# Performance work log

Hardware: AMD Instinct MI355X
Metric: run time of the kernel (lower is better)

Reference implementation:

```python
import jax, jax.numpy as jnp
import numpy as np

NUM_TRAITS = 5
NUM_MODALITIES = 3
K = 8
EPS = 1e-08


def setup_inputs() -> dict:
    key = jax.random.key(0)
    k1, k2, k3, k4 = jax.random.split(key, 4)
    labeled_embeddings = jax.random.normal(k1, (20000, NUM_MODALITIES, 256), dtype=jnp.float32)
    labeled_traits = jax.random.uniform(k2, (20000, NUM_TRAITS), dtype=jnp.float32)
    unlabeled_embeddings = jax.random.normal(k3, (2048, NUM_MODALITIES, 256), dtype=jnp.float32)
    trait_modality_logits = jax.random.normal(k4, (NUM_TRAITS, NUM_MODALITIES), dtype=jnp.float32)
    return {
        'labeled_embeddings': labeled_embeddings,
        'labeled_traits': labeled_traits,
        'unlabeled_embeddings': unlabeled_embeddings,
        'trait_modality_logits': trait_modality_logits,
    }


def reference(labeled_embeddings, labeled_traits, unlabeled_embeddings, trait_modality_logits):
    # L2-normalize along feature dim (eps added to norm, matching torch code)
    lab_norm = labeled_embeddings / (jnp.linalg.norm(labeled_embeddings, axis=-1, keepdims=True) + EPS)
    unl_norm = unlabeled_embeddings / (jnp.linalg.norm(unlabeled_embeddings, axis=-1, keepdims=True) + EPS)

    # per-modality cosine similarity: [U, M, L]
    modality_sim = jnp.einsum('umd,lmd->uml', unl_norm, lab_norm)

    # per-trait modality weights and weighted similarity: [U, T, L]
    modality_weights = jax.nn.softmax(trait_modality_logits, axis=-1)  # [T, M]
    combined_sim = jnp.einsum('tm,uml->utl', modality_weights, modality_sim)

    # top-k neighbors per (query, trait)
    _, neighbor_indices = jax.lax.top_k(combined_sim, K)  # [U, T, K]

    # gather modality embeddings for neighbors: [U, T, K, M, D]
    neighbor_embeddings = labeled_embeddings[neighbor_indices]

    # gather the trait value corresponding to each trait head: [U, T, K]
    trait_ids = jnp.arange(NUM_TRAITS)[None, :, None]  # [1, T, 1]
    neighbor_traits = labeled_traits[neighbor_indices, trait_ids]

    return neighbor_embeddings, neighbor_traits, neighbor_indices.astype(jnp.int64)
```

## Files before the change

kernel.cpp:

```cpp
#include <hip/hip_runtime.h>
#include <hip/hip_bf16.h>
#include <math.h>

#define L_CNT 20000
#define U_CNT 2048
#define M_CNT 3
#define D_CNT 256
#define KTOT  768
#define T_CNT 5
#define K_OUT 8
#define KC    16
#define LP    20096
#define LROWS (L_CNT*M_CNT)
#define UROWS (U_CNT*M_CNT)
#define CHUNKS 313
#define CPAD   320

typedef unsigned short ushort_t;
typedef unsigned int uint_t;
typedef __attribute__((ext_vector_type(8))) short bf16x8;
typedef __attribute__((ext_vector_type(4))) float f32x4;

__device__ inline double dshfl_xor(double v, int m){
    long long x = __double_as_longlong(v);
    int lo = (int)(x & 0xffffffffLL);
    int hi = (int)(((unsigned long long)x) >> 32);
    lo = __shfl_xor(lo, m, 64);
    hi = __shfl_xor(hi, m, 64);
    return __longlong_as_double(((long long)hi << 32) | (long long)(unsigned int)lo);
}
__device__ inline unsigned short f2bf(float f){
    unsigned int u = __float_as_uint(f);
    u = (u + 0x7fffu + ((u >> 16) & 1u)) >> 16;
    return (unsigned short)u;
}
__device__ __forceinline__ void gload16(const void* g, void* l){
    __builtin_amdgcn_global_load_lds(
        (const __attribute__((address_space(1))) unsigned int*)g,
        (__attribute__((address_space(3))) unsigned int*)l, 16, 0, 0);
}
__device__ __forceinline__ float h2f(ushort_t h){
    _Float16 x; __builtin_memcpy(&x, &h, 2); return (float)x;
}
__device__ __forceinline__ ushort_t f2h(float f){
    _Float16 hv = (_Float16)f;
    ushort_t b; __builtin_memcpy(&b, &hv, 2);
    return b;
}
__device__ __forceinline__ ushort_t f2key(float f){
    ushort_t b = f2h(f);
    ushort_t mask = (ushort_t)(0x8000u | (((short)b >> 15) & 0x7FFF));
    return (ushort_t)(b ^ mask);
}
__device__ __forceinline__ ushort_t get16(const uint4& v, int e){
    uint_t w = (e < 2) ? v.x : (e < 4) ? v.y : (e < 6) ? v.z : v.w;
    return (ushort_t)((e & 1) ? (w >> 16) : (w & 0xFFFFu));
}
__device__ __forceinline__ ushort_t u2get(const uint2& v, int e){
    uint_t w = (e < 2) ? v.x : v.y;
    return (ushort_t)((e & 1) ? (w >> 16) : (w & 0xFFFFu));
}
__device__ __forceinline__ float comb3(float w0, float w1, float w2, float a, float b, float c){
    return fmaf(w2, c, fmaf(w1, b, w0*a));
}
__device__ __forceinline__ void radix_find(uint_t hist[4][256], uint_t* h1, uint_t* h2,
    int tid, uint_t addBase, uint_t kc, uint_t* shB, uint_t* shAbove)
{
    h1[tid] = hist[0][tid]+hist[1][tid]+hist[2][tid]+hist[3][tid];
    uint_t* src = h1; uint_t* dst = h2;
    for (int st=1; st<256; st<<=1){
        __syncthreads();
        dst[tid] = src[tid] + ((tid+st < 256) ? src[tid+st] : 0u);
        uint_t* tt = src; src = dst; dst = tt;
    }
    __syncthreads();
    uint_t ge = src[tid] + addBase;
    uint_t gt = ((tid < 255) ? src[tid+1] : 0u) + addBase;
    if (ge >= kc && gt < kc){ *shB = (uint_t)tid; *shAbove = gt; }
    __syncthreads();
}

__global__ void weights_kernel(const float* __restrict__ logits,
                               float* __restrict__ w32, double* __restrict__ w64){
    int t = threadIdx.x;
    if (t < T_CNT){
        float a = logits[t*M_CNT+0], b = logits[t*M_CNT+1], c = logits[t*M_CNT+2];
        float mx = fmaxf(a, fmaxf(b, c));
        float e0 = expf(a-mx), e1 = expf(b-mx), e2 = expf(c-mx);
        float s = e0+e1+e2;
        w32[t*M_CNT+0] = e0/s; w32[t*M_CNT+1] = e1/s; w32[t*M_CNT+2] = e2/s;
        double da=(double)a, db=(double)b, dc=(double)c;
        double dmx = fmax(da, fmax(db, dc));
        double f0 = exp(da-dmx), f1 = exp(db-dmx), f2 = exp(dc-dmx);
        double ds = f0+f1+f2;
        w64[t*M_CNT+0] = f0/ds; w64[t*M_CNT+1] = f1/ds; w64[t*M_CNT+2] = f2/ds;
    }
}

__global__ __launch_bounds__(256) void prep_kernel(const float* __restrict__ lab,
    const float* __restrict__ unl, double* __restrict__ invL64, double* __restrict__ invU64,
    ushort_t* __restrict__ labN, ushort_t* __restrict__ unlN){
    const int NROW = LROWS + UROWS;
    int row = blockIdx.x*4 + (threadIdx.x >> 6);
    int lane = threadIdx.x & 63;
    if (row >= NROW) return;
    bool isLab = row < LROWS;
    const float* p = isLab ? (lab + (size_t)row*D_CNT) : (unl + (size_t)(row-LROWS)*D_CNT);
    float4 a = ((const float4*)p)[lane];
    double sS = (double)a.x*a.x + (double)a.y*a.y + (double)a.z*a.z + (double)a.w*a.w;
#pragma unroll
    for (int m=1;m<64;m<<=1) sS += dshfl_xor(sS, m);
    double inv = 1.0/(sqrt(sS) + 1e-8);
    if (lane == 0){
        if (isLab) invL64[row] = inv;
        else invU64[row-LROWS] = inv;
    }
    float sc = (float)inv;
    ushort4 o;
    o.x = f2bf(a.x*sc); o.y = f2bf(a.y*sc); o.z = f2bf(a.z*sc); o.w = f2bf(a.w*sc);
    ushort_t* dst = isLab ? (labN + (size_t)row*D_CNT) : (unlN + (size_t)(row-LROWS)*D_CNT);
    *(ushort4*)&dst[lane*4] = o;
}

__global__ __launch_bounds__(256, 2) void sim_kernel(
    const ushort_t* __restrict__ labN, const ushort_t* __restrict__ unlN,
    const float* __restrict__ w32, ushort_t* __restrict__ slabp,
    ushort_t* __restrict__ chunkMax)
{
    __shared__ ushort_t sA[128][64];
    __shared__ ushort_t sB[128][64];

    const int tid  = threadIdx.x;
    const int lane = tid & 63;
    const int w    = tid >> 6;
    const int wu = w >> 1, wl = w & 1;
    const int fr = lane & 15, fg = lane >> 4;

    const int uB = blockIdx.x * 128;
    const int l0 = blockIdx.y * 128;

    const int sr   = lane >> 3;
    const int scol = ((lane & 7) ^ sr) * 8;
    const ushort_t* pA[4]; const ushort_t* pB[4];
    ushort_t* dA[4]; ushort_t* dB[4];
#pragma unroll
    for (int g=0; g<4; g++){
        int ar = uB + g*32 + w*8 + sr;
        pA[g] = unlN + (size_t)ar*KTOT + scol;
        dA[g] = &sA[g*32 + w*8][0];
        int br = l0 + g*32 + w*8 + sr; if (br > L_CNT-1) br = L_CNT-1;
        pB[g] = labN + (size_t)br*KTOT + scol;
        dB[g] = &sB[g*32 + w*8][0];
    }

    int aoff[4][2], boff[4][2];
#pragma unroll
    for (int i=0;i<4;i++)
#pragma unroll
        for (int ks=0;ks<2;ks++){
            int sw = ((ks*4 + fg) ^ (fr & 7)) * 16;
            aoff[i][ks] = (wu*64 + i*16 + fr)*128 + sw;
            boff[i][ks] = (wl*64 + i*16 + fr)*128 + sw;
        }

    uint2 hA[4][4], hB[4][4];

#pragma unroll
    for (int m=0; m<M_CNT; m++){
        f32x4 acc[4][4];
#pragma unroll
        for (int i=0;i<4;i++)
#pragma unroll
            for (int j=0;j<4;j++) acc[i][j] = (f32x4){0.f,0.f,0.f,0.f};

#pragma unroll
        for (int kb=0; kb<4; kb++){
            const int koff = (m*4 + kb) * 64;
            __syncthreads();
#pragma unroll
            for (int g=0; g<4; g++){
                gload16(pA[g] + koff, dA[g]);
                gload16(pB[g] + koff, dB[g]);
            }
            __syncthreads();
#pragma unroll
            for (int ks=0; ks<2; ks++){
                bf16x8 af[4], bf[4];
#pragma unroll
                for (int i=0;i<4;i++) af[i] = *(const bf16x8*)((const char*)sA + aoff[i][ks]);
#pragma unroll
                for (int j=0;j<4;j++) bf[j] = *(const bf16x8*)((const char*)sB + boff[j][ks]);
#pragma unroll
                for (int i=0;i<4;i++)
#pragma unroll
                    for (int j=0;j<4;j++)
                        acc[i][j] = __builtin_amdgcn_mfma_f32_16x16x32_bf16(bf[j], af[i], acc[i][j], 0, 0, 0);
            }
        }

        float wl5[T_CNT][3];
        uint_t rm[4][T_CNT];
        if (m == 2){
#pragma unroll
            for (int t=0;t<T_CNT;t++){
#pragma unroll
                for (int j=0;j<3;j++) wl5[t][j] = w32[t*3+j];
#pragma unroll
                for (int i=0;i<4;i++) rm[i][t] = 0;
            }
        }
#pragma unroll
        for (int i=0;i<4;i++){
            const int u = uB + wu*64 + i*16 + fr;
            const size_t rowbase = ((size_t)u*M_CNT + m)*LP;
#pragma unroll
            for (int j=0;j<4;j++){
                const int l = l0 + wl*64 + j*16 + fg*4;
                uint2 hp;
                hp.x = (uint_t)f2h(acc[i][j][0]) | ((uint_t)f2h(acc[i][j][1]) << 16);
                hp.y = (uint_t)f2h(acc[i][j][2]) | ((uint_t)f2h(acc[i][j][3]) << 16);
                *(uint2*)&slabp[rowbase + l] = hp;
                if (m == 0) hA[i][j] = hp;
                else if (m == 1) hB[i][j] = hp;
                else {
#pragma unroll
                    for (int e=0;e<4;e++){
                        if (l + e < L_CNT){
                            float av = h2f(u2get(hA[i][j], e));
                            float bv = h2f(u2get(hB[i][j], e));
                            float cv = h2f(u2get(hp, e));
#pragma unroll
                            for (int t=0;t<T_CNT;t++){
                                uint_t k = f2key(comb3(wl5[t][0],wl5[t][1],wl5[t][2], av,bv,cv));
                                rm[i][t] = (k > rm[i][t]) ? k : rm[i][t];
                            }
                        }
                    }
                }
            }
        }
        if (m == 2){
#pragma unroll
            for (int i=0;i<4;i++)
#pragma unroll
                for (int t=0;t<T_CNT;t++){
                    uint_t k = rm[i][t], o;
                    o = (uint_t)__shfl_xor((int)k, 16, 64); k = (o > k) ? o : k;
                    o = (uint_t)__shfl_xor((int)k, 32, 64); k = (o > k) ? o : k;
                    rm[i][t] = k;
                }
            if (fg == 0){
                int chunkc = (l0 >> 6) + wl;
                if (chunkc < CHUNKS){
#pragma unroll
                    for (int i=0;i<4;i++){
                        int u = uB + wu*64 + i*16 + fr;
#pragma unroll
                        for (int t=0;t<T_CNT;t++)
                            chunkMax[((size_t)u*T_CNT + t)*CPAD + chunkc] = (ushort_t)rm[i][t];
                    }
                }
            }
        }
    }
}

__global__ __launch_bounds__(256) void select2_kernel(
    const ushort_t* __restrict__ slabp, const ushort_t* __restrict__ chunkMax,
    const float* __restrict__ w32, int* __restrict__ candIdx)
{
    __shared__ ushort_t mxs[CPAD];
    __shared__ ushort_t cand[CPAD];
    __shared__ uint_t hist[4][256];
    __shared__ uint_t h1[256], h2[256];
    __shared__ uint_t shB, shAbove, shNc, shCtr0, shCtr1;
    __shared__ int bufc[KC];

    const int tid = threadIdx.x, wid = tid >> 6;
    const int u = blockIdx.x, t = blockIdx.y;
    const float w0 = w32[t*3+0], w1 = w32[t*3+1], w2 = w32[t*3+2];
    const ushort_t* s0 = slabp + ((size_t)u*M_CNT + 0)*LP;
    const ushort_t* s1 = slabp + ((size_t)u*M_CNT + 1)*LP;
    const ushort_t* s2 = slabp + ((size_t)u*M_CNT + 2)*LP;
    const ushort_t* cm = chunkMax + ((size_t)u*T_CNT + t)*CPAD;

    for (int i=tid; i<CPAD; i+=256) mxs[i] = (i < CHUNKS) ? cm[i] : (ushort_t)0;
    hist[0][tid]=0; hist[1][tid]=0; hist[2][tid]=0; hist[3][tid]=0;
    if (tid == 0){ shNc = 0; shCtr0 = 0; shCtr1 = 0; }
    __syncthreads();

    for (int i=tid; i<CHUNKS; i+=256) atomicAdd(&hist[wid][mxs[i] >> 8], 1u);
    __syncthreads();
    radix_find(hist, h1, h2, tid, 0u, KC, &shB, &shAbove);
    const uint_t MB = shB, mAb = shAbove;
    hist[0][tid]=0; hist[1][tid]=0; hist[2][tid]=0; hist[3][tid]=0;
    __syncthreads();
    for (int i=tid; i<CHUNKS; i+=256){
        uint_t k = mxs[i];
        if ((k >> 8) == MB) atomicAdd(&hist[wid][k & 0xFFu], 1u);
    }
    __syncthreads();
    radix_find(hist, h1, h2, tid, mAb, KC, &shB, &shAbove);
    const uint_t tau = (MB << 8) | shB;
    hist[0][tid]=0; hist[1][tid]=0; hist[2][tid]=0; hist[3][tid]=0;
    __syncthreads();

    for (int i=tid; i<CHUNKS; i+=256)
        if ((uint_t)mxs[i] >= tau) cand[atomicAdd(&shNc, 1u)] = (ushort_t)i;
    __syncthreads();
    const int NE = (int)shNc * 64;

    for (int j=tid; j<NE; j+=256){
        int l = (int)cand[j>>6]*64 + (j & 63);
        if (l < L_CNT){
            uint_t k = f2key(comb3(w0,w1,w2, h2f(s0[l]), h2f(s1[l]), h2f(s2[l])));
            atomicAdd(&hist[wid][k >> 8], 1u);
        }
    }
    __syncthreads();
    radix_find(hist, h1, h2, tid, 0u, KC, &shB, &shAbove);
    const uint_t EB = shB, eAb = shAbove;
    hist[0][tid]=0; hist[1][tid]=0; hist[2][tid]=0; hist[3][tid]=0;
    __syncthreads();

    for (int j=tid; j<NE; j+=256){
        int l = (int)cand[j>>6]*64 + (j & 63);
        if (l < L_CNT){
            uint_t k = f2key(comb3(w0,w1,w2, h2f(s0[l]), h2f(s1[l]), h2f(s2[l])));
            if ((k >> 8) == EB) atomicAdd(&hist[wid][k & 0xFFu], 1u);
        }
    }
    __syncthreads();
    radix_find(hist, h1, h2, tid, eAb, KC, &shB, &shAbove);
    const uint_t K16 = (EB << 8) | shB;
    const uint_t tot = shAbove;

    for (int j=tid; j<NE; j+=256){
        int l = (int)cand[j>>6]*64 + (j & 63);
        if (l < L_CNT){
            uint_t k = f2key(comb3(w0,w1,w2, h2f(s0[l]), h2f(s1[l]), h2f(s2[l])));
            if (k > K16){
                bufc[atomicAdd(&shCtr0, 1u)] = l;
            } else if (k == K16){
                uint_t s = atomicAdd(&shCtr1, 1u) + tot;
                if (s < (uint_t)KC) bufc[s] = l;
            }
        }
    }
    __syncthreads();
    if (tid < KC) candIdx[((size_t)u*T_CNT + t)*KC + tid] = bufc[tid];
}

__global__ __launch_bounds__(256) void rescore_kernel(
    const float* __restrict__ lab, const float* __restrict__ unl,
    const double* __restrict__ w64, const double* __restrict__ invL64,
    const double* __restrict__ invU64, const int* __restrict__ candIdx,
    double* __restrict__ candSim)
{
    int q = blockIdx.x*4 + (threadIdx.x >> 6);
    int lane = threadIdx.x & 63;
    int ut = q >> 4;
    int t = ut % T_CNT;
    int u = ut / T_CNT;
    int idx = candIdx[q];
    double sim = 0.0;
#pragma unroll
    for (int m=0;m<M_CNT;m++){
        float4 a = *(const float4*)&unl[(((size_t)u*M_CNT)+m)*D_CNT + lane*4];
        float4 b = *(const float4*)&lab[(((size_t)idx*M_CNT)+m)*D_CNT + lane*4];
        double d = (double)a.x*b.x + (double)a.y*b.y + (double)a.z*b.z + (double)a.w*b.w;
#pragma unroll
        for (int mm=1;mm<64;mm<<=1) d += dshfl_xor(d, mm);
        sim += w64[t*M_CNT+m] * d * invU64[u*M_CNT+m] * invL64[idx*M_CNT+m];
    }
    if (lane == 0) candSim[q] = sim;
}

__global__ __launch_bounds__(256) void finalize_kernel(
    const double* __restrict__ candSim, const int* __restrict__ candIdx,
    const float* __restrict__ traits,
    float* __restrict__ outTraits, float* __restrict__ outIdx, int* __restrict__ finalIdx)
{
    int id = blockIdx.x*256 + threadIdx.x;
    if (id >= U_CNT*T_CNT) return;
    int t = id % T_CNT;
    double cv[KC]; int ci[KC];
#pragma unroll
    for (int c=0;c<KC;c++){ cv[c] = candSim[(size_t)id*KC + c]; ci[c] = candIdx[(size_t)id*KC + c]; }
#pragma unroll
    for (int i=0;i<KC;i++)
#pragma unroll
        for (int j=0;j<KC-1;j++){
            bool sw = (cv[j] < cv[j+1]) || (cv[j] == cv[j+1] && ci[j] > ci[j+1]);
            if (sw){ double tv=cv[j]; cv[j]=cv[j+1]; cv[j+1]=tv; int ti=ci[j]; ci[j]=ci[j+1]; ci[j+1]=ti; }
        }
#pragma unroll
    for (int k=0;k<K_OUT;k++){
        size_t ob = (size_t)id*K_OUT + k;
        int fi = ci[k];
        outTraits[ob] = traits[(size_t)fi*T_CNT + t];
        outIdx[ob] = (float)fi;
        finalIdx[ob] = fi;
    }
}

__global__ __launch_bounds__(192) void gather_kernel(const float* __restrict__ lab,
    const int* __restrict__ finalIdx, float* __restrict__ outEmb)
{
    int b = blockIdx.x;
    int idx = finalIdx[b];
    const float4* src = (const float4*)(lab + (size_t)idx * (M_CNT*D_CNT));
    float4* dst = (float4*)(outEmb + (size_t)b * (M_CNT*D_CNT));
    dst[threadIdx.x] = src[threadIdx.x];
}

extern "C" void kernel_launch(void* const* d_in, const int* in_sizes, int n_in,
                              void* d_out, int out_size, void* d_ws, size_t ws_size,
                              hipStream_t stream) {
    const float* lab    = (const float*)d_in[0];
    const float* traits = (const float*)d_in[1];
    const float* unl    = (const float*)d_in[2];
    const float* logits = (const float*)d_in[3];

    float* out = (float*)d_out;
    float* outEmb = out;
    float* outTr  = out + (size_t)U_CNT*T_CNT*K_OUT*M_CNT*D_CNT;
    float* outIx  = outTr + (size_t)U_CNT*T_CNT*K_OUT;

    char* wsb = (char*)d_ws;
    size_t off = 0;
    auto take = [&](size_t bytes)->void*{
        void* p = wsb + off;
        off = (off + bytes + 255) & ~(size_t)255;
        return p;
    };
    double* invL64 = (double*)take((size_t)LROWS*sizeof(double));
    double* invU64 = (double*)take((size_t)UROWS*sizeof(double));
    float*  w32    = (float*) take(T_CNT*M_CNT*sizeof(float));
    double* w64    = (double*)take(T_CNT*M_CNT*sizeof(double));
    int*    candIdx= (int*)   take((size_t)U_CNT*T_CNT*KC*sizeof(int));
    double* candSim= (double*)take((size_t)U_CNT*T_CNT*KC*sizeof(double));
    int*    finalIdx=(int*)   take((size_t)U_CNT*T_CNT*K_OUT*sizeof(int));
    ushort_t* labN = (ushort_t*)take((size_t)LROWS*D_CNT*sizeof(ushort_t));
    ushort_t* unlN = (ushort_t*)take((size_t)UROWS*D_CNT*sizeof(ushort_t));
    ushort_t* chunkMax = (ushort_t*)take((size_t)U_CNT*T_CNT*CPAD*sizeof(ushort_t));

    ushort_t* slabV = (ushort_t*)outEmb;

    weights_kernel<<<1, 64, 0, stream>>>(logits, w32, w64);
    {
        int nrow = LROWS + UROWS;
        prep_kernel<<<(nrow+3)/4, 256, 0, stream>>>(lab, unl, invL64, invU64, labN, unlN);
    }
    sim_kernel<<<dim3(U_CNT/128, (L_CNT + 127)/128), 256, 0, stream>>>(labN, unlN, w32, slabV, chunkMax);
    select2_kernel<<<dim3(U_CNT, T_CNT), 256, 0, stream>>>(slabV, chunkMax, w32, candIdx);
    rescore_kernel<<<(U_CNT*T_CNT*KC)/4, 256, 0, stream>>>(lab, unl, w64, invL64, invU64, candIdx, candSim);
    finalize_kernel<<<(U_CNT*T_CNT + 255)/256, 256, 0, stream>>>(candSim, candIdx, traits, outTr, outIx, finalIdx);
    gather_kernel<<<U_CNT*T_CNT*K_OUT, 192, 0, stream>>>(lab, finalIdx, outEmb);
}
```

Baseline: 463.6 us.

## Double-buffer LDS tiles in similarity GEMM to overlap loads with MFMA

The similarity kernel now keeps two LDS buffers for the A and B tiles. It issues the global-to-LDS copies for the next 64-wide k slice before running the MFMAs on the current slice, so memory latency can hide behind compute. The three per-modality loops are flattened into one 12-step loop with a single barrier per step instead of two, and the fp16 store and chunk-max epilogue run every fourth step. LDS use per block doubles, which may limit occupancy or change register pressure.

```diff
diff --git a/kernel.cpp b/kernel.cpp
--- a/kernel.cpp
+++ b/kernel.cpp
@@ -51,10 +51,6 @@
     ushort_t b = f2h(f);
     ushort_t mask = (ushort_t)(0x8000u | (((short)b >> 15) & 0x7FFF));
     return (ushort_t)(b ^ mask);
-}
-__device__ __forceinline__ ushort_t get16(const uint4& v, int e){
-    uint_t w = (e < 2) ? v.x : (e < 4) ? v.y : (e < 6) ? v.z : v.w;
-    return (ushort_t)((e & 1) ? (w >> 16) : (w & 0xFFFFu));
 }
 __device__ __forceinline__ ushort_t u2get(const uint2& v, int e){
     uint_t w = (e < 2) ? v.x : v.y;
@@ -127,8 +123,8 @@
     const float* __restrict__ w32, ushort_t* __restrict__ slabp,
     ushort_t* __restrict__ chunkMax)
 {
-    __shared__ ushort_t sA[128][64];
-    __shared__ ushort_t sB[128][64];
+    __shared__ ushort_t sA[2][128][64];
+    __shared__ ushort_t sB[2][128][64];
 
     const int tid  = threadIdx.x;
     const int lane = tid & 63;
@@ -142,15 +138,17 @@
     const int sr   = lane >> 3;
     const int scol = ((lane & 7) ^ sr) * 8;
     const ushort_t* pA[4]; const ushort_t* pB[4];
-    ushort_t* dA[4]; ushort_t* dB[4];
+    ushort_t* dA0[4]; ushort_t* dA1[4]; ushort_t* dB0[4]; ushort_t* dB1[4];
 #pragma unroll
     for (int g=0; g<4; g++){
         int ar = uB + g*32 + w*8 + sr;
         pA[g] = unlN + (size_t)ar*KTOT + scol;
-        dA[g] = &sA[g*32 + w*8][0];
+        dA0[g] = &sA[0][g*32 + w*8][0];
+        dA1[g] = &sA[1][g*32 + w*8][0];
         int br = l0 + g*32 + w*8 + sr; if (br > L_CNT-1) br = L_CNT-1;
         pB[g] = labN + (size_t)br*KTOT + scol;
-        dB[g] = &sB[g*32 + w*8][0];
+        dB0[g] = &sB[0][g*32 + w*8][0];
+        dB1[g] = &sB[1][g*32 + w*8][0];
     }
 
     int aoff[4][2], boff[4][2];
@@ -165,31 +163,40 @@
 
     uint2 hA[4][4], hB[4][4];
 
-#pragma unroll
-    for (int m=0; m<M_CNT; m++){
-        f32x4 acc[4][4];
-#pragma unroll
-        for (int i=0;i<4;i++)
-#pragma unroll
-            for (int j=0;j<4;j++) acc[i][j] = (f32x4){0.f,0.f,0.f,0.f};
-
-#pragma unroll
-        for (int kb=0; kb<4; kb++){
-            const int koff = (m*4 + kb) * 64;
-            __syncthreads();
+    f32x4 acc[4][4];
+#pragma unroll
+    for (int i=0;i<4;i++)
+#pragma unroll
+        for (int j=0;j<4;j++) acc[i][j] = (f32x4){0.f,0.f,0.f,0.f};
+
+#pragma unroll
+    for (int g=0; g<4; g++){
+        gload16(pA[g], dA0[g]);
+        gload16(pB[g], dB0[g]);
+    }
+    __syncthreads();
+
+#pragma unroll
+    for (int t=0; t<12; ++t){
+        const int cur = t & 1;
+        if (t < 11){
+            const int koff = (t+1)*64;
 #pragma unroll
             for (int g=0; g<4; g++){
-                gload16(pA[g] + koff, dA[g]);
-                gload16(pB[g] + koff, dB[g]);
-            }
-            __syncthreads();
+                gload16(pA[g] + koff, cur ? dA0[g] : dA1[g]);
+                gload16(pB[g] + koff, cur ? dB0[g] : dB1[g]);
+            }
+        }
+        {
+            const char* baseA = (const char*)sA + cur*16384;
+            const char* baseB = (const char*)sB + cur*16384;
 #pragma unroll
             for (int ks=0; ks<2; ks++){
                 bf16x8 af[4], bf[4];
 #pragma unroll
-                for (int i=0;i<4;i++) af[i] = *(const bf16x8*)((const char*)sA + aoff[i][ks]);
-#pragma unroll
-                for (int j=0;j<4;j++) bf[j] = *(const bf16x8*)((const char*)sB + boff[j][ks]);
+                for (int i=0;i<4;i++) af[i] = *(const bf16x8*)(baseA + aoff[i][ks]);
+#pragma unroll
+                for (int j=0;j<4;j++) bf[j] = *(const bf16x8*)(baseB + boff[j][ks]);
 #pragma unroll
                 for (int i=0;i<4;i++)
 #pragma unroll
@@ -197,71 +204,78 @@
                         acc[i][j] = __builtin_amdgcn_mfma_f32_16x16x32_bf16(bf[j], af[i], acc[i][j], 0, 0, 0);
             }
         }
-
-        float wl5[T_CNT][3];
-        uint_t rm[4][T_CNT];
-        if (m == 2){
-#pragma unroll
-            for (int t=0;t<T_CNT;t++){
-#pragma unroll
-                for (int j=0;j<3;j++) wl5[t][j] = w32[t*3+j];
-#pragma unroll
-                for (int i=0;i<4;i++) rm[i][t] = 0;
-            }
-        }
-#pragma unroll
-        for (int i=0;i<4;i++){
-            const int u = uB + wu*64 + i*16 + fr;
-            const size_t rowbase = ((size_t)u*M_CNT + m)*LP;
-#pragma unroll
-            for (int j=0;j<4;j++){
-                const int l = l0 + wl*64 + j*16 + fg*4;
-                uint2 hp;
-                hp.x = (uint_t)f2h(acc[i][j][0]) | ((uint_t)f2h(acc[i][j][1]) << 16);
-                hp.y = (uint_t)f2h(acc[i][j][2]) | ((uint_t)f2h(acc[i][j][3]) << 16);
-                *(uint2*)&slabp[rowbase + l] = hp;
-                if (m == 0) hA[i][j] = hp;
-                else if (m == 1) hB[i][j] = hp;
-                else {
-#pragma unroll
-                    for (int e=0;e<4;e++){
-                        if (l + e < L_CNT){
-                            float av = h2f(u2get(hA[i][j], e));
-                            float bv = h2f(u2get(hB[i][j], e));
-                            float cv = h2f(u2get(hp, e));
-#pragma unroll
-                            for (int t=0;t<T_CNT;t++){
-                                uint_t k = f2key(comb3(wl5[t][0],wl5[t][1],wl5[t][2], av,bv,cv));
-                                rm[i][t] = (k > rm[i][t]) ? k : rm[i][t];
+        if ((t & 3) == 3){
+            const int m = t >> 2;
+            float wl5[T_CNT][3];
+            uint_t rm[4][T_CNT];
+            if (m == 2){
+#pragma unroll
+                for (int tt=0;tt<T_CNT;tt++){
+#pragma unroll
+                    for (int j=0;j<3;j++) wl5[tt][j] = w32[tt*3+j];
+#pragma unroll
+                    for (int i=0;i<4;i++) rm[i][tt] = 0;
+                }
+            }
+#pragma unroll
+            for (int i=0;i<4;i++){
+                const int u = uB + wu*64 + i*16 + fr;
+                const size_t rowbase = ((size_t)u*M_CNT + m)*LP;
+#pragma unroll
+                for (int j=0;j<4;j++){
+                    const int l = l0 + wl*64 + j*16 + fg*4;
+                    uint2 hp;
+                    hp.x = (uint_t)f2h(acc[i][j][0]) | ((uint_t)f2h(acc[i][j][1]) << 16);
+                    hp.y = (uint_t)f2h(acc[i][j][2]) | ((uint_t)f2h(acc[i][j][3]) << 16);
+                    *(uint2*)&slabp[rowbase + l] = hp;
+                    if (m == 0) hA[i][j] = hp;
+                    else if (m == 1) hB[i][j] = hp;
+                    else {
+#pragma unroll
+                        for (int e=0;e<4;e++){
+                            if (l + e < L_CNT){
+                                float av = h2f(u2get(hA[i][j], e));
+                                float bv = h2f(u2get(hB[i][j], e));
+                                float cv = h2f(u2get(hp, e));
+#pragma unroll
+                                for (int tt=0;tt<T_CNT;tt++){
+                                    uint_t k = f2key(comb3(wl5[tt][0],wl5[tt][1],wl5[tt][2], av,bv,cv));
+                                    rm[i][tt] = (k > rm[i][tt]) ? k : rm[i][tt];
+                                }
                             }
                         }
                     }
                 }
             }
-        }
-        if (m == 2){
-#pragma unroll
-            for (int i=0;i<4;i++)
-#pragma unroll
-                for (int t=0;t<T_CNT;t++){
-                    uint_t k = rm[i][t], o;
-                    o = (uint_t)__shfl_xor((int)k, 16, 64); k = (o > k) ? o : k;
-                    o = (uint_t)__shfl_xor((int)k, 32, 64); k = (o > k) ? o : k;
-                    rm[i][t] = k;
-                }
-            if (fg == 0){
-                int chunkc = (l0 >> 6) + wl;
-                if (chunkc < CHUNKS){
-#pragma unroll
-                    for (int i=0;i<4;i++){
-                        int u = uB + wu*64 + i*16 + fr;
-#pragma unroll
-                        for (int t=0;t<T_CNT;t++)
-                            chunkMax[((size_t)u*T_CNT + t)*CPAD + chunkc] = (ushort_t)rm[i][t];
+            if (m == 2){
+#pragma unroll
+                for (int i=0;i<4;i++)
+#pragma unroll
+                    for (int tt=0;tt<T_CNT;tt++){
+                        uint_t k = rm[i][tt], o;
+                        o = (uint_t)__shfl_xor((int)k, 16, 64); k = (o > k) ? o : k;
+                        o = (uint_t)__shfl_xor((int)k, 32, 64); k = (o > k) ? o : k;
+                        rm[i][tt] = k;
+                    }
+                if (fg == 0){
+                    int chunkc = (l0 >> 6) + wl;
+                    if (chunkc < CHUNKS){
+#pragma unroll
+                        for (int i=0;i<4;i++){
+                            int u = uB + wu*64 + i*16 + fr;
+#pragma unroll
+                            for (int tt=0;tt<T_CNT;tt++)
+                                chunkMax[((size_t)u*T_CNT + tt)*CPAD + chunkc] = (ushort_t)rm[i][tt];
+                        }
                     }
                 }
             }
-        }
+#pragma unroll
+            for (int i=0;i<4;i++)
+#pragma unroll
+                for (int j=0;j<4;j++) acc[i][j] = (f32x4){0.f,0.f,0.f,0.f};
+        }
+        __syncthreads();
     }
 }
 
```

New measurement: 465.6 us. About the same (+0.4%).
